# Optimization experiments

Hardware: AMD Instinct MI355X
Metric: run time of the kernel (lower is better)

The kernel has to match this reference:

```python
import jax, jax.numpy as jnp
import numpy as np

DEGREE = 3
N_KNOTS = 5

def _bspline_basis(x, t_ext, degree):
    """Vectorized Cox-de Boor. x: (..., ), t_ext: (m,) extended knots.
    Returns (..., m-1-degree) degree-`degree` basis values."""
    xe = x[..., None]
    # order-0 indicator basis: (..., m-1)
    B = ((xe >= t_ext[:-1]) & (xe < t_ext[1:])).astype(x.dtype)
    for p in range(1, degree + 1):
        left_den = t_ext[p:-1] - t_ext[:-(p + 1)]
        right_den = t_ext[p + 1:] - t_ext[1:-p]
        left = jnp.where(left_den > 0,
                         (xe - t_ext[:-(p + 1)]) / jnp.where(left_den > 0, left_den, 1.0),
                         0.0) * B[..., :-1]
        right = jnp.where(right_den > 0,
                          (t_ext[p + 1:] - xe) / jnp.where(right_den > 0, right_den, 1.0),
                          0.0) * B[..., 1:]
        B = left + right
    return B

def setup_inputs() -> dict:
    key = jax.random.key(0)
    k1, k2, k3, k4 = jax.random.split(key, 4)
    batch, input_dim, out_dim = 16384, 4096, 64
    n_coeff = N_KNOTS - DEGREE  # 2
    return {
        "x": jax.random.normal(k1, (batch, input_dim), dtype=jnp.float32),
        "c": jax.random.normal(k2, (input_dim, out_dim, n_coeff), dtype=jnp.float32),
        "ws": jax.random.normal(k3, (input_dim, out_dim), dtype=jnp.float32),
        "wb": jax.random.normal(k4, (input_dim, out_dim), dtype=jnp.float32),
    }

def reference(x, c, ws, wb):
    t = jnp.linspace(-1.0, 1.0, N_KNOTS, dtype=x.dtype)
    t_ext = jnp.concatenate([t, t[-1:]])  # pad so basis count == n_knots - degree
    # B: (batch, input_dim, n_coeff); basis depends only on x, shared knots
    B = _bspline_basis(x, t_ext, DEGREE)
    spline = jnp.einsum('bik,ijk->bj', B, c * ws[:, :, None])
    silu_mix = jax.nn.silu(x) @ wb  # sum_i wb[i,j] * x_i*sigmoid(x_i)
    return spline + silu_mix
```

## Files before the change

kernel.cpp:

```cpp
#include <hip/hip_runtime.h>
#include <hip/hip_bf16.h>
#include <stdint.h>

#define BATCH   16384
#define IN_DIM  4096
#define OUT_DIM 64
#define KI      64
#define KCH     (3*KI)
#define LDSTR   (KCH+8)
#define NCHUNK  (IN_DIM/KI)
#define SPLITK  4
#define CPB     (NCHUNK/SPLITK)
#define MTILES  (BATCH/64)

typedef __attribute__((ext_vector_type(8))) short   short8;
typedef __attribute__((ext_vector_type(4))) float   floatx4;
typedef __attribute__((ext_vector_type(4))) uint32_t uintx4;

static __device__ __forceinline__ unsigned short f2bf(float f) {
    union { float f; uint32_t u; } v; v.f = f;
    uint32_t r = v.u + 0x7FFFu + ((v.u >> 16) & 1u);
    return (unsigned short)(r >> 16);
}

static __device__ __forceinline__ void kan_features(float xv, float& b0, float& b1, float& sl) {
    float ax = fabsf(xv);
    float om = 1.0f - ax;
    float inner = (4.0f*ax - 4.0f)*(ax*ax) + (2.0f/3.0f);
    float outer = (4.0f/3.0f)*om*om*om;
    b0 = (ax < 0.5f) ? inner : outer;
    b0 = (ax < 1.0f) ? b0 : 0.0f;
    float c3  = (xv < 0.0f) ? (4.0f/3.0f) : (-14.0f/3.0f);
    float mid = ((c3*xv + 2.0f)*xv + 1.0f)*xv + (1.0f/6.0f);
    float hi  = (((22.0f*xv - 48.0f)*xv + 30.0f)*xv - 4.0f) * (1.0f/3.0f);
    b1 = (xv < 0.5f) ? mid : hi;
    b1 = (xv >= -0.5f && xv < 1.0f) ? b1 : 0.0f;
    float e = __expf(-xv);
    sl = xv * __builtin_amdgcn_rcpf(1.0f + e);
}

__global__ __launch_bounds__(256) void kan_prep(
        const float* __restrict__ c, const float* __restrict__ ws,
        const float* __restrict__ wb, unsigned short* __restrict__ Wt) {
    int idx = blockIdx.x * 256 + threadIdx.x;
    int row = idx >> 9;
    int i   = (idx & 511) << 3;
    int j   = row / 3;
    int t   = row - j*3;
    int ci  = i >> 6, il = i & 63;
    unsigned short pk[8];
    #pragma unroll
    for (int e = 0; e < 8; e++) {
        int ii = i + e;
        float v;
        if (t < 2) v = c[(size_t)ii*(OUT_DIM*2) + j*2 + t] * ws[(size_t)ii*OUT_DIM + j];
        else       v = wb[(size_t)ii*OUT_DIM + j];
        pk[e] = f2bf(v);
    }
    uintx4 d;
    d[0] = pk[0] | ((uint32_t)pk[1] << 16);
    d[1] = pk[2] | ((uint32_t)pk[3] << 16);
    d[2] = pk[4] | ((uint32_t)pk[5] << 16);
    d[3] = pk[6] | ((uint32_t)pk[7] << 16);
    *(uintx4*)(Wt + (size_t)((ci*64 + j)*3 + t)*KI + il) = d;
}

template<bool PRE>
__global__ __launch_bounds__(256) void kan_main(
    const float* __restrict__ x, const float* __restrict__ c,
    const float* __restrict__ ws, const float* __restrict__ wb,
    const unsigned short* __restrict__ Wt, float* __restrict__ out)
{
    __shared__ unsigned short Bs[OUT_DIM * LDSTR];

    const int tid  = threadIdx.x;
    const int wave = tid >> 6;
    const int lane = tid & 63;
    const int m    = lane & 15;
    const int q    = lane >> 4;
    const int mt   = blockIdx.x & (MTILES - 1);
    const int kh   = blockIdx.x >> 8;
    const int row0 = mt * 64;
    const int r    = row0 + wave*16 + m;
    const float* xrow = x + (size_t)r * IN_DIM;

    floatx4 acc[4] = {};

    for (int cc = 0; cc < CPB; cc++) {
        const int ci = kh * CPB + cc;
        const int i0 = ci * KI;

        __syncthreads();

        if (PRE) {
            const unsigned short* gW = Wt + (size_t)ci * (OUT_DIM * KCH);
            #pragma unroll
            for (int p = 0; p < 6; p++) {
                int seg = tid + p*256;
                uintx4 d = *(const uintx4*)(gW + seg*8);
                int j = seg / 24;
                *(uintx4*)&Bs[seg*8 + j*8] = d;
            }
        } else {
            #pragma unroll
            for (int p = 0; p < 16; p++) {
                int idx = tid + p*256;
                int j = idx & 63, i = idx >> 6;
                int gi = i0 + i;
                const float* cp = c + ((size_t)gi*OUT_DIM + j)*2;
                float c0 = cp[0], c1 = cp[1];
                float s  = ws[(size_t)gi*OUT_DIM + j];
                float b  = wb[(size_t)gi*OUT_DIM + j];
                Bs[j*LDSTR + i]        = f2bf(c0*s);
                Bs[j*LDSTR + KI + i]   = f2bf(c1*s);
                Bs[j*LDSTR + 2*KI + i] = f2bf(b);
            }
        }

        floatx4 xv[4];
        xv[0] = *(const floatx4*)(xrow + i0 + q*8);
        xv[1] = *(const floatx4*)(xrow + i0 + q*8 + 4);
        xv[2] = *(const floatx4*)(xrow + i0 + 32 + q*8);
        xv[3] = *(const floatx4*)(xrow + i0 + 32 + q*8 + 4);

        short8 af[6];
        #pragma unroll
        for (int g = 0; g < 2; g++) {
            #pragma unroll
            for (int e = 0; e < 8; e++) {
                float v = xv[g*2 + (e >> 2)][e & 3];
                float b0, b1, sl;
                kan_features(v, b0, b1, sl);
                af[0 + g][e] = (short)f2bf(b0);
                af[2 + g][e] = (short)f2bf(b1);
                af[4 + g][e] = (short)f2bf(sl);
            }
        }

        __syncthreads();

        #pragma unroll
        for (int s = 0; s < 6; s++) {
            #pragma unroll
            for (int n = 0; n < 4; n++) {
                short8 bf = *(const short8*)&Bs[(n*16 + m)*LDSTR + s*32 + q*8];
                acc[n] = __builtin_amdgcn_mfma_f32_16x16x32_bf16(af[s], bf, acc[n], 0, 0, 0);
            }
        }
    }

    #pragma unroll
    for (int n = 0; n < 4; n++) {
        #pragma unroll
        for (int reg = 0; reg < 4; reg++) {
            int orow = row0 + wave*16 + q*4 + reg;
            atomicAdd(&out[(size_t)orow*OUT_DIM + n*16 + m], acc[n][reg]);
        }
    }
}

extern "C" void kernel_launch(void* const* d_in, const int* in_sizes, int n_in,
                              void* d_out, int out_size, void* d_ws, size_t ws_size,
                              hipStream_t stream) {
    const float* x  = (const float*)d_in[0];
    const float* c  = (const float*)d_in[1];
    const float* ws = (const float*)d_in[2];
    const float* wb = (const float*)d_in[3];
    float* out = (float*)d_out;

    hipMemsetAsync(d_out, 0, (size_t)out_size * sizeof(float), stream);

    const size_t need = (size_t)OUT_DIM * 3 * IN_DIM * 2;
    if (ws_size >= need) {
        kan_prep<<<384, 256, 0, stream>>>(c, ws, wb, (unsigned short*)d_ws);
        kan_main<true><<<MTILES * SPLITK, 256, 0, stream>>>(
            x, c, ws, wb, (const unsigned short*)d_ws, out);
    } else {
        kan_main<false><<<MTILES * SPLITK, 256, 0, stream>>>(
            x, c, ws, wb, (const unsigned short*)d_ws, out);
    }
}
```

Before: 413.8 us.

## Prefetch next x chunk and weights into registers, XOR-swizzle LDS layout

Measured after the change: 403.5 us. 1.03x faster.

```diff
diff --git a/kernel.cpp b/kernel.cpp
--- a/kernel.cpp
+++ b/kernel.cpp
@@ -7,11 +7,11 @@
 #define OUT_DIM 64
 #define KI      64
 #define KCH     (3*KI)
-#define LDSTR   (KCH+8)
 #define NCHUNK  (IN_DIM/KI)
 #define SPLITK  4
 #define CPB     (NCHUNK/SPLITK)
 #define MTILES  (BATCH/64)
+#define CHW     (OUT_DIM*KCH)
 
 typedef __attribute__((ext_vector_type(8))) short   short8;
 typedef __attribute__((ext_vector_type(4))) float   floatx4;
@@ -25,14 +25,15 @@
 
 static __device__ __forceinline__ void kan_features(float xv, float& b0, float& b1, float& sl) {
     float ax = fabsf(xv);
+    float a2 = ax*ax;
     float om = 1.0f - ax;
-    float inner = (4.0f*ax - 4.0f)*(ax*ax) + (2.0f/3.0f);
-    float outer = (4.0f/3.0f)*om*om*om;
+    float inner = __builtin_fmaf(__builtin_fmaf(4.0f, ax, -4.0f), a2, (2.0f/3.0f));
+    float outer = (om*om) * (om * (4.0f/3.0f));
     b0 = (ax < 0.5f) ? inner : outer;
     b0 = (ax < 1.0f) ? b0 : 0.0f;
     float c3  = (xv < 0.0f) ? (4.0f/3.0f) : (-14.0f/3.0f);
-    float mid = ((c3*xv + 2.0f)*xv + 1.0f)*xv + (1.0f/6.0f);
-    float hi  = (((22.0f*xv - 48.0f)*xv + 30.0f)*xv - 4.0f) * (1.0f/3.0f);
+    float mid = __builtin_fmaf(__builtin_fmaf(__builtin_fmaf(c3, xv, 2.0f), xv, 1.0f), xv, (1.0f/6.0f));
+    float hi  = __builtin_fmaf(__builtin_fmaf(__builtin_fmaf(22.0f, xv, -48.0f), xv, 30.0f), xv, -4.0f) * (1.0f/3.0f);
     b1 = (xv < 0.5f) ? mid : hi;
     b1 = (xv >= -0.5f && xv < 1.0f) ? b1 : 0.0f;
     float e = __expf(-xv);
@@ -47,7 +48,7 @@
     int i   = (idx & 511) << 3;
     int j   = row / 3;
     int t   = row - j*3;
-    int ci  = i >> 6, il = i & 63;
+    int ci  = i >> 6, il0 = i & 63;
     unsigned short pk[8];
     #pragma unroll
     for (int e = 0; e < 8; e++) {
@@ -62,16 +63,17 @@
     d[1] = pk[2] | ((uint32_t)pk[3] << 16);
     d[2] = pk[4] | ((uint32_t)pk[5] << 16);
     d[3] = pk[6] | ((uint32_t)pk[7] << 16);
-    *(uintx4*)(Wt + (size_t)((ci*64 + j)*3 + t)*KI + il) = d;
+    int g = j*24 + (((t << 3) | (il0 >> 3)) ^ (j & 7));
+    *(uintx4*)(Wt + (size_t)ci*CHW + g*8) = d;
 }
 
 template<bool PRE>
-__global__ __launch_bounds__(256) void kan_main(
+__global__ __launch_bounds__(256, 4) void kan_main(
     const float* __restrict__ x, const float* __restrict__ c,
     const float* __restrict__ ws, const float* __restrict__ wb,
     const unsigned short* __restrict__ Wt, float* __restrict__ out)
 {
-    __shared__ unsigned short Bs[OUT_DIM * LDSTR];
+    __shared__ unsigned short Bs[CHW];
 
     const int tid  = threadIdx.x;
     const int wave = tid >> 6;
@@ -86,21 +88,52 @@
 
     floatx4 acc[4] = {};
 
+    const int i00 = kh * CPB * KI;
+    floatx4 xv[4];
+    xv[0] = *(const floatx4*)(xrow + i00 + q*8);
+    xv[1] = *(const floatx4*)(xrow + i00 + q*8 + 4);
+    xv[2] = *(const floatx4*)(xrow + i00 + 32 + q*8);
+    xv[3] = *(const floatx4*)(xrow + i00 + 32 + q*8 + 4);
+
     for (int cc = 0; cc < CPB; cc++) {
         const int ci = kh * CPB + cc;
         const int i0 = ci * KI;
 
+        uintx4 stg[6];
+        if (PRE) {
+            const unsigned short* gW = Wt + (size_t)ci * CHW;
+            #pragma unroll
+            for (int p = 0; p < 6; p++)
+                stg[p] = *(const uintx4*)(gW + (tid + p*256)*8);
+        }
+
+        const int inx = (cc + 1 < CPB) ? (i0 + KI) : i0;
+        floatx4 xvn[4];
+        xvn[0] = *(const floatx4*)(xrow + inx + q*8);
+        xvn[1] = *(const floatx4*)(xrow + inx + q*8 + 4);
+        xvn[2] = *(const floatx4*)(xrow + inx + 32 + q*8);
+        xvn[3] = *(const floatx4*)(xrow + inx + 32 + q*8 + 4);
+
+        short8 af[6];
+        #pragma unroll
+        for (int g = 0; g < 2; g++) {
+            #pragma unroll
+            for (int e = 0; e < 8; e++) {
+                float v = xv[g*2 + (e >> 2)][e & 3];
+                float b0, b1, sl;
+                kan_features(v, b0, b1, sl);
+                af[0 + g][e] = (short)f2bf(b0);
+                af[2 + g][e] = (short)f2bf(b1);
+                af[4 + g][e] = (short)f2bf(sl);
+            }
+        }
+
         __syncthreads();
 
         if (PRE) {
-            const unsigned short* gW = Wt + (size_t)ci * (OUT_DIM * KCH);
-            #pragma unroll
-            for (int p = 0; p < 6; p++) {
-                int seg = tid + p*256;
-                uintx4 d = *(const uintx4*)(gW + seg*8);
-                int j = seg / 24;
-                *(uintx4*)&Bs[seg*8 + j*8] = d;
-            }
+            #pragma unroll
+            for (int p = 0; p < 6; p++)
+                *(uintx4*)&Bs[(tid + p*256)*8] = stg[p];
         } else {
             #pragma unroll
             for (int p = 0; p < 16; p++) {
@@ -111,29 +144,10 @@
                 float c0 = cp[0], c1 = cp[1];
                 float s  = ws[(size_t)gi*OUT_DIM + j];
                 float b  = wb[(size_t)gi*OUT_DIM + j];
-                Bs[j*LDSTR + i]        = f2bf(c0*s);
-                Bs[j*LDSTR + KI + i]   = f2bf(c1*s);
-                Bs[j*LDSTR + 2*KI + i] = f2bf(b);
-            }
-        }
-
-        floatx4 xv[4];
-        xv[0] = *(const floatx4*)(xrow + i0 + q*8);
-        xv[1] = *(const floatx4*)(xrow + i0 + q*8 + 4);
-        xv[2] = *(const floatx4*)(xrow + i0 + 32 + q*8);
-        xv[3] = *(const floatx4*)(xrow + i0 + 32 + q*8 + 4);
-
-        short8 af[6];
-        #pragma unroll
-        for (int g = 0; g < 2; g++) {
-            #pragma unroll
-            for (int e = 0; e < 8; e++) {
-                float v = xv[g*2 + (e >> 2)][e & 3];
-                float b0, b1, sl;
-                kan_features(v, b0, b1, sl);
-                af[0 + g][e] = (short)f2bf(b0);
-                af[2 + g][e] = (short)f2bf(b1);
-                af[4 + g][e] = (short)f2bf(sl);
+                int jx = j & 7;
+                Bs[j*KCH + ((0*8 + (i>>3)) ^ jx)*8 + (i&7)] = f2bf(c0*s);
+                Bs[j*KCH + ((1*8 + (i>>3)) ^ jx)*8 + (i&7)] = f2bf(c1*s);
+                Bs[j*KCH + ((2*8 + (i>>3)) ^ jx)*8 + (i&7)] = f2bf(b);
             }
         }
 
@@ -141,12 +155,16 @@
 
         #pragma unroll
         for (int s = 0; s < 6; s++) {
+            const int kb = (s >> 1)*8 + (s & 1)*4 + q;
             #pragma unroll
             for (int n = 0; n < 4; n++) {
-                short8 bf = *(const short8*)&Bs[(n*16 + m)*LDSTR + s*32 + q*8];
+                const int j = n*16 + m;
+                short8 bf = *(const short8*)&Bs[j*KCH + ((kb ^ (j & 7)) << 3)];
                 acc[n] = __builtin_amdgcn_mfma_f32_16x16x32_bf16(af[s], bf, acc[n], 0, 0, 0);
             }
         }
+
+        xv[0] = xvn[0]; xv[1] = xvn[1]; xv[2] = xvn[2]; xv[3] = xvn[3];
     }
 
     #pragma unroll
@@ -170,7 +188,7 @@
 
     hipMemsetAsync(d_out, 0, (size_t)out_size * sizeof(float), stream);
 
-    const size_t need = (size_t)OUT_DIM * 3 * IN_DIM * 2;
+    const size_t need = (size_t)NCHUNK * CHW * sizeof(unsigned short);
     if (ws_size >= need) {
         kan_prep<<<384, 256, 0, stream>>>(c, ws, wb, (unsigned short*)d_ws);
         kan_main<true><<<MTILES * SPLITK, 256, 0, stream>>>(
```
